# Performance work log

Measured on AMD Instinct MI355X. Metric: run time of the kernel, lower is better.

The kernel has to match this reference:

```python
import jax, jax.numpy as jnp
import numpy as np

H_GRU = 32  # GRU hidden size fixed to 32 in the module


def setup_inputs() -> dict:
    key = jax.random.key(0)
    ks = jax.random.split(key, 12)
    B, C_in, H, W = 64, 64, 48, 160
    C_out = 64
    s_in = 1.0 / np.sqrt(C_in)
    s_h = 1.0 / np.sqrt(H_GRU)
    u = lambda k, shape: jax.random.uniform(k, shape, jnp.float32, -s_h, s_h)
    return {
        "x": jax.random.normal(ks[0], (B, C_in, H, W), jnp.float32),
        "conv_w": jax.random.normal(ks[1], (C_out, C_in), jnp.float32) * s_in,
        "conv_b": jax.random.normal(ks[2], (C_out,), jnp.float32) * s_in,
        "wih_f": u(ks[3], (3 * H_GRU, C_out)),
        "whh_f": u(ks[4], (3 * H_GRU, H_GRU)),
        "bih_f": u(ks[5], (3 * H_GRU,)),
        "bhh_f": u(ks[6], (3 * H_GRU,)),
        "wih_b": u(ks[7], (3 * H_GRU, C_out)),
        "whh_b": u(ks[8], (3 * H_GRU, H_GRU)),
        "bih_b": u(ks[9], (3 * H_GRU,)),
        "bhh_b": u(ks[10], (3 * H_GRU,)),
    }


def _gru_scan(pre, whh, bhh):
    # pre: [N, T, 3H] input-side gate pre-activations (already x@Wih^T + bih)
    N = pre.shape[0]

    def step(h, g):
        gh = h @ whh.T + bhh
        gi_r, gi_z, gi_n = jnp.split(g, 3, axis=-1)
        gh_r, gh_z, gh_n = jnp.split(gh, 3, axis=-1)
        r = jax.nn.sigmoid(gi_r + gh_r)
        z = jax.nn.sigmoid(gi_z + gh_z)
        n = jnp.tanh(gi_n + r * gh_n)
        h_new = (1.0 - z) * n + z * h
        return h_new, h_new

    h0 = jnp.zeros((N, H_GRU), pre.dtype)
    _, ys = jax.lax.scan(step, h0, jnp.swapaxes(pre, 0, 1))  # ys: [T, N, H]
    return jnp.swapaxes(ys, 0, 1)  # [N, T, H]


def reference(x, conv_w, conv_b, wih_f, whh_f, bih_f, bhh_f,
              wih_b, whh_b, bih_b, bhh_b):
    B, C_in, H, W = x.shape
    # 1x1 conv fused with the NCHW->NHWC permute
    y = jnp.einsum('bchw,oc->bhwo', x, conv_w) + conv_b  # [B, H, W, C_out]
    C_out = y.shape[-1]
    seq = y.reshape(B * H, W, C_out)  # GRU batch = B*H, seq_len = W
    # forward direction
    pre_f = jnp.einsum('ntc,gc->ntg', seq, wih_f) + bih_f
    out_f = _gru_scan(pre_f, whh_f, bhh_f)
    # backward direction: scan reversed sequence, then flip output back
    seq_r = seq[:, ::-1, :]
    pre_b = jnp.einsum('ntc,gc->ntg', seq_r, wih_b) + bih_b
    out_b = _gru_scan(pre_b, whh_b, bhh_b)[:, ::-1, :]
    out = jnp.concatenate([out_f, out_b], axis=-1)  # [B*H, W, 2*H_GRU]
    out = out.reshape(B, H, W, 2 * H_GRU)
    return jnp.transpose(out, (0, 3, 1, 2))  # back to NCHW
```

## Files before the change

kernel.cpp:

```cpp
#include <hip/hip_runtime.h>


typedef _Float16 f16x8 __attribute__((ext_vector_type(8)));
typedef _Float16 f16x4 __attribute__((ext_vector_type(4)));
typedef float f32x4 __attribute__((ext_vector_type(4)));

#define HWSTRIDE 7680
#define NCHUNK 10

#define WS_BIAS_OFF 24576

__global__ void fold_weights(const float* __restrict__ conv_w,
                             const float* __restrict__ conv_b,
                             const float* __restrict__ wih_f,
                             const float* __restrict__ bih_f,
                             const float* __restrict__ bhh_f,
                             const float* __restrict__ wih_b,
                             const float* __restrict__ bih_b,
                             const float* __restrict__ bhh_b,
                             void* wsv)
{
    _Float16* W2 = (_Float16*)wsv;
    float* bias = (float*)((char*)wsv + WS_BIAS_OFF);
    const int idx = blockIdx.x * 256 + threadIdx.x;
    if (idx < 12288) {
        const int d = idx / 6144, r = idx % 6144, g = r / 64, c = r % 64;
        const float* wih = d ? wih_b : wih_f;
        float acc = 0.f;
        for (int o = 0; o < 64; ++o) acc += wih[g * 64 + o] * conv_w[o * 64 + c];
        W2[idx] = (_Float16)acc;
    } else if (idx < 12288 + 256) {
        const int e = idx - 12288;
        const int d = e >> 7, rr = e & 127, kind = rr >> 5, j = rr & 31;
        const float* wih = d ? wih_b : wih_f;
        const float* bih = d ? bih_b : bih_f;
        const float* bhh = d ? bhh_b : bhh_f;
        float v;
        if (kind == 0 || kind == 1) {
            const int g = j + kind * 32;
            float b2 = bih[g];
            for (int o = 0; o < 64; ++o) b2 += wih[g * 64 + o] * conv_b[o];
            v = b2 + bhh[g];
        } else if (kind == 2) {
            const int g = j + 64;
            float b2 = bih[g];
            for (int o = 0; o < 64; ++o) b2 += wih[g * 64 + o] * conv_b[o];
            v = b2;
        } else {
            v = bhh[j + 64];
        }
        bias[(d * 4 + kind) * 32 + j] = v;
    }
}

__global__ __launch_bounds__(128, 3)
void gru_fused3(const float* __restrict__ x,
                const float* __restrict__ whh_f,
                const float* __restrict__ whh_b,
                const void* __restrict__ wsv,
                float* __restrict__ out)
{
    __shared__ __align__(16) _Float16 xt[2][2][64][16];
    __shared__ __align__(16) _Float16 s_pre[2][16][2][100];
    __shared__ __align__(16) float s_h[64];

    const int n    = blockIdx.x;
    const int b    = n / 48;
    const int h    = n % 48;
    const int lane = threadIdx.x & 63;
    const int wave = threadIdx.x >> 6;
    const int sw   = blockIdx.x & 1;
    const float* xbase = x + (size_t)b * (64 * HWSTRIDE) + (size_t)h * 160;

    if (wave == sw) {
        const int d0 = lane >> 5, j = lane & 31;
        const float* whh = d0 ? whh_b : whh_f;
        float w[96];
        #pragma unroll
        for (int g3 = 0; g3 < 3; ++g3)
            #pragma unroll
            for (int k4 = 0; k4 < 8; ++k4) {
                const float4 wv = *(const float4*)&whh[(j + 32 * g3) * 32 + k4 * 4];
                w[g3 * 32 + k4 * 4 + 0] = wv.x; w[g3 * 32 + k4 * 4 + 1] = wv.y;
                w[g3 * 32 + k4 * 4 + 2] = wv.z; w[g3 * 32 + k4 * 4 + 3] = wv.w;
            }
        const float* bias = (const float*)((const char*)wsv + WS_BIAS_OFF);
        const float bc_r = bias[(d0 * 4 + 0) * 32 + j];
        const float bc_z = bias[(d0 * 4 + 1) * 32 + j];
        const float b2n  = bias[(d0 * 4 + 2) * 32 + j];
        const float bhn  = bias[(d0 * 4 + 3) * 32 + j];
        float* orow = out + (((size_t)b * 64 + (size_t)(d0 * 32 + j)) * 48 + h) * 160;

        s_h[lane] = 0.f;
        float hcur = 0.f;
        __syncthreads();

        for (int ci = 0; ci < NCHUNK; ++ci) {
            const int buf = ci & 1;
            float hh[16];
            #pragma unroll
            for (int tq = 0; tq < 16; ++tq) {
                const float pr = (float)s_pre[buf][tq][d0][j];
                const float pz = (float)s_pre[buf][tq][d0][j + 32];
                const float pn = (float)s_pre[buf][tq][d0][j + 64];
                float4 hq[8];
                #pragma unroll
                for (int q = 0; q < 8; ++q) hq[q] = ((const float4*)&s_h[d0 * 32])[q];
                const float* hv = (const float*)hq;
                float ar = bc_r, az = bc_z, an = bhn;
                float ar2 = 0.f, az2 = 0.f, an2 = 0.f;
                #pragma unroll
                for (int k = 0; k < 32; k += 2) {
                    const float h0 = hv[k], h1 = hv[k + 1];
                    ar  = fmaf(w[k],      h0, ar );
                    az  = fmaf(w[32 + k], h0, az );
                    an  = fmaf(w[64 + k], h0, an );
                    ar2 = fmaf(w[k + 1],      h1, ar2);
                    az2 = fmaf(w[33 + k],     h1, az2);
                    an2 = fmaf(w[65 + k],     h1, an2);
                }
                const float gr = (ar + ar2) + pr;
                const float gz = (az + az2) + pz;
                const float gn = an + an2;
                const float r = __builtin_amdgcn_rcpf(1.f + __expf(-gr));
                const float z = __builtin_amdgcn_rcpf(1.f + __expf(-gz));
                float ta = (pn + b2n) + r * gn;
                ta = fminf(fmaxf(ta, -15.f), 15.f);
                const float e2 = __expf(2.f * ta);
                const float nn = (e2 - 1.f) * __builtin_amdgcn_rcpf(e2 + 1.f);
                hcur = (1.f - z) * nn + z * hcur;
                s_h[lane] = hcur;
                asm volatile("" ::: "memory");
                hh[tq] = hcur;
            }
            if (d0 == 0) {
                #pragma unroll
                for (int q = 0; q < 4; ++q)
                    *(float4*)&orow[ci * 16 + q * 4] =
                        make_float4(hh[q*4], hh[q*4+1], hh[q*4+2], hh[q*4+3]);
            } else {
                const int base = 144 - ci * 16;
                #pragma unroll
                for (int q = 0; q < 4; ++q)
                    *(float4*)&orow[base + q * 4] =
                        make_float4(hh[15-q*4], hh[14-q*4], hh[13-q*4], hh[12-q*4]);
            }
            __syncthreads();
        }
    } else {
        const _Float16* W2 = (const _Float16*)wsv;
        const int t  = lane & 15;
        const int g8 = (lane >> 4) * 8;
        const int g4 = (lane >> 4) * 4;
        f16x8 A[2][6][2];
        #pragma unroll
        for (int d = 0; d < 2; ++d)
            #pragma unroll
            for (int gt = 0; gt < 6; ++gt)
                #pragma unroll
                for (int kt = 0; kt < 2; ++kt)
                    A[d][gt][kt] = *(const f16x8*)&W2[(d * 96 + gt * 16 + t) * 64 + kt * 32 + g8];

        const int sc = lane >> 2, stq = lane & 3;

        auto stage_dir = [&](int cc, int d, float4* v, bool issue) {
            const int w0 = d ? (144 - cc * 16) : (cc * 16);
            if (issue) {
                #pragma unroll
                for (int k = 0; k < 4; ++k)
                    v[k] = *(const float4*)(xbase + (size_t)(sc + 16 * k) * HWSTRIDE + w0 + stq * 4);
            } else {
                #pragma unroll
                for (int k = 0; k < 4; ++k) {
                    f16x4 p;
                    p[0] = (_Float16)v[k].x; p[1] = (_Float16)v[k].y;
                    p[2] = (_Float16)v[k].z; p[3] = (_Float16)v[k].w;
                    *(f16x4*)&xt[cc & 1][d][sc + 16 * k][stq * 4] = p;
                }
            }
        };
        auto project_dir = [&](int cn, int d) {
            const int buf = cn & 1;
            const _Float16* xr = &xt[buf][d][0][0];
            f16x8 bf0, bf1;
            #pragma unroll
            for (int e = 0; e < 8; ++e) {
                bf0[e] = xr[(g8 + e) * 16 + t];
                bf1[e] = xr[(32 + g8 + e) * 16 + t];
            }
            const int row = d ? (15 - t) : t;
            #pragma unroll
            for (int gt = 0; gt < 6; ++gt) {
                f32x4 acc = {0.f, 0.f, 0.f, 0.f};
                acc = __builtin_amdgcn_mfma_f32_16x16x32_f16(A[d][gt][0], bf0, acc, 0, 0, 0);
                acc = __builtin_amdgcn_mfma_f32_16x16x32_f16(A[d][gt][1], bf1, acc, 0, 0, 0);
                f16x4 o;
                o[0] = (_Float16)acc[0]; o[1] = (_Float16)acc[1];
                o[2] = (_Float16)acc[2]; o[3] = (_Float16)acc[3];
                *(f16x4*)&s_pre[buf][row][d][gt * 16 + g4] = o;
            }
        };

        {
            float4 v[4];
            stage_dir(0, 0, v, true);  stage_dir(0, 0, v, false);
            stage_dir(0, 1, v, true);  stage_dir(0, 1, v, false);
            stage_dir(1, 0, v, true);  stage_dir(1, 0, v, false);
            stage_dir(1, 1, v, true);  stage_dir(1, 1, v, false);
            project_dir(0, 0);
            project_dir(0, 1);
        }
        __syncthreads();

        for (int ci = 0; ci < NCHUNK; ++ci) {
            const int cn = ci + 1, cs = ci + 2;
            float4 va[4], vb[4];
            if (cs < NCHUNK) stage_dir(cs, 0, va, true);
            if (cn < NCHUNK) project_dir(cn, 0);
            if (cs < NCHUNK) { stage_dir(cs, 0, va, false); stage_dir(cs, 1, vb, true); }
            if (cn < NCHUNK) project_dir(cn, 1);
            if (cs < NCHUNK) stage_dir(cs, 1, vb, false);
            __syncthreads();
        }
    }
}

extern "C" void kernel_launch(void* const* d_in, const int* in_sizes, int n_in,
                              void* d_out, int out_size, void* d_ws, size_t ws_size,
                              hipStream_t stream) {
    (void)in_sizes; (void)n_in; (void)ws_size; (void)out_size;
    fold_weights<<<dim3(49), dim3(256), 0, stream>>>(
        (const float*)d_in[1],
        (const float*)d_in[2],
        (const float*)d_in[3],
        (const float*)d_in[5],
        (const float*)d_in[6],
        (const float*)d_in[7],
        (const float*)d_in[9],
        (const float*)d_in[10],
        d_ws);
    gru_fused3<<<dim3(3072), dim3(128), 0, stream>>>(
        (const float*)d_in[0],
        (const float*)d_in[4],
        (const float*)d_in[8],
        d_ws,
        (float*)d_out);
}
```

Measured before the change: 186.9 us.

## Split GRU into single-wave blocks per direction with K-split recurrence

Replaces the two-wave block (one recurrence wave plus one projection/staging wave) with one 64-lane block per sequence and direction, which doubles the grid. Each block stages its own input and runs its own MFMA projection between chunks. The recurrent matvec is split over two half-waves, each summing half of K, and the halves are combined with a cross-lane shuffle. This halves the register weights per lane and removes the block barriers. The cost is that projection now runs serially with the recurrence inside one wave instead of overlapping with it, and f16 conversion now uses packed RTZ.

```diff
diff --git a/kernel.cpp b/kernel.cpp
--- a/kernel.cpp
+++ b/kernel.cpp
@@ -2,12 +2,11 @@
 
 
 typedef _Float16 f16x8 __attribute__((ext_vector_type(8)));
-typedef _Float16 f16x4 __attribute__((ext_vector_type(4)));
+typedef __fp16   pk16  __attribute__((ext_vector_type(2)));
 typedef float f32x4 __attribute__((ext_vector_type(4)));
 
 #define HWSTRIDE 7680
 #define NCHUNK 10
-
 #define WS_BIAS_OFF 24576
 
 __global__ void fold_weights(const float* __restrict__ conv_w,
@@ -53,174 +52,155 @@
     }
 }
 
-__global__ __launch_bounds__(128, 3)
-void gru_fused3(const float* __restrict__ x,
+__global__ __launch_bounds__(64, 3)
+void gru_fused4(const float* __restrict__ x,
                 const float* __restrict__ whh_f,
                 const float* __restrict__ whh_b,
                 const void* __restrict__ wsv,
                 float* __restrict__ out)
 {
-    __shared__ __align__(16) _Float16 xt[2][2][64][16];
-    __shared__ __align__(16) _Float16 s_pre[2][16][2][100];
-    __shared__ __align__(16) float s_h[64];
-
-    const int n    = blockIdx.x;
+    __shared__ __align__(16) _Float16 xt[64][18];
+    __shared__ __align__(16) _Float16 s_pre[16][104];
+    __shared__ __align__(16) float s_h[32];
+
+    const int d    = blockIdx.x & 1;
+    const int n    = blockIdx.x >> 1;
     const int b    = n / 48;
     const int h    = n % 48;
-    const int lane = threadIdx.x & 63;
-    const int wave = threadIdx.x >> 6;
-    const int sw   = blockIdx.x & 1;
+    const int lane = threadIdx.x;
+    const int kh   = lane >> 5;
+    const int j    = lane & 31;
+    const int t16  = lane & 15;
+    const int g8   = (lane >> 4) * 8;
+    const int sc   = lane >> 2;
+    const int stq  = lane & 3;
+
     const float* xbase = x + (size_t)b * (64 * HWSTRIDE) + (size_t)h * 160;
 
-    if (wave == sw) {
-        const int d0 = lane >> 5, j = lane & 31;
-        const float* whh = d0 ? whh_b : whh_f;
-        float w[96];
-        #pragma unroll
-        for (int g3 = 0; g3 < 3; ++g3)
+    const _Float16* W2 = (const _Float16*)wsv + (size_t)d * 96 * 64;
+    f16x8 A[6][2];
+    #pragma unroll
+    for (int gt = 0; gt < 6; ++gt)
+        #pragma unroll
+        for (int kt = 0; kt < 2; ++kt)
+            A[gt][kt] = *(const f16x8*)&W2[(gt * 16 + t16) * 64 + kt * 32 + g8];
+
+    const float* whh = d ? whh_b : whh_f;
+    float w[48];
+    #pragma unroll
+    for (int g = 0; g < 3; ++g)
+        #pragma unroll
+        for (int q = 0; q < 4; ++q) {
+            const float4 wv = *(const float4*)&whh[(j + 32 * g) * 32 + kh * 16 + q * 4];
+            w[g * 16 + q * 4 + 0] = wv.x; w[g * 16 + q * 4 + 1] = wv.y;
+            w[g * 16 + q * 4 + 2] = wv.z; w[g * 16 + q * 4 + 3] = wv.w;
+        }
+    const float* bias = (const float*)((const char*)wsv + WS_BIAS_OFF);
+    const float bc_r = bias[(d * 4 + 0) * 32 + j];
+    const float bc_z = bias[(d * 4 + 1) * 32 + j];
+    const float b2n  = bias[(d * 4 + 2) * 32 + j];
+    const float bhn  = bias[(d * 4 + 3) * 32 + j];
+
+    float* orow = out + (((size_t)b * 64 + (size_t)(d * 32 + j)) * 48 + h) * 160;
+
+    float4 pf[4];
+    auto issue_pf = [&](int cc) {
+        const int w0 = d ? (144 - cc * 16) : (cc * 16);
+        #pragma unroll
+        for (int k = 0; k < 4; ++k)
+            pf[k] = *(const float4*)(xbase + (size_t)(sc + 16 * k) * HWSTRIDE + w0 + stq * 4);
+    };
+    auto write_xt = [&]() {
+        #pragma unroll
+        for (int k = 0; k < 4; ++k) {
+            pk16 lo = __builtin_amdgcn_cvt_pkrtz(pf[k].x, pf[k].y);
+            pk16 hi = __builtin_amdgcn_cvt_pkrtz(pf[k].z, pf[k].w);
+            *(pk16*)&xt[sc + 16 * k][stq * 4]     = lo;
+            *(pk16*)&xt[sc + 16 * k][stq * 4 + 2] = hi;
+        }
+    };
+    auto project = [&]() {
+        f16x8 bf0, bf1;
+        #pragma unroll
+        for (int e = 0; e < 8; ++e) {
+            bf0[e] = xt[g8 + e][t16];
+            bf1[e] = xt[32 + g8 + e][t16];
+        }
+        const int row = d ? (15 - t16) : t16;
+        #pragma unroll
+        for (int gt = 0; gt < 6; ++gt) {
+            f32x4 acc = {0.f, 0.f, 0.f, 0.f};
+            acc = __builtin_amdgcn_mfma_f32_16x16x32_f16(A[gt][0], bf0, acc, 0, 0, 0);
+            acc = __builtin_amdgcn_mfma_f32_16x16x32_f16(A[gt][1], bf1, acc, 0, 0, 0);
+            pk16 o0 = __builtin_amdgcn_cvt_pkrtz(acc[0], acc[1]);
+            pk16 o1 = __builtin_amdgcn_cvt_pkrtz(acc[2], acc[3]);
+            *(pk16*)&s_pre[row][gt * 16 + (lane >> 4) * 4]     = o0;
+            *(pk16*)&s_pre[row][gt * 16 + (lane >> 4) * 4 + 2] = o1;
+        }
+    };
+
+    issue_pf(0);
+    write_xt();
+    issue_pf(1);
+    project();
+    if (kh == 0) s_h[j] = 0.f;
+    float hcur = 0.f;
+
+    for (int ci = 0; ci < NCHUNK; ++ci) {
+        float hh[8];
+        #pragma unroll
+        for (int s = 0; s < 16; ++s) {
+            const float pr = (float)s_pre[s][j];
+            const float pz = (float)s_pre[s][j + 32];
+            const float pn = (float)s_pre[s][j + 64];
+            float4 h4[4];
             #pragma unroll
-            for (int k4 = 0; k4 < 8; ++k4) {
-                const float4 wv = *(const float4*)&whh[(j + 32 * g3) * 32 + k4 * 4];
-                w[g3 * 32 + k4 * 4 + 0] = wv.x; w[g3 * 32 + k4 * 4 + 1] = wv.y;
-                w[g3 * 32 + k4 * 4 + 2] = wv.z; w[g3 * 32 + k4 * 4 + 3] = wv.w;
+            for (int q = 0; q < 4; ++q) h4[q] = ((const float4*)&s_h[16 * kh])[q];
+            const float* hv = (const float*)h4;
+            float ar0 = 0.f, az0 = 0.f, an0 = 0.f;
+            float ar1 = 0.f, az1 = 0.f, an1 = 0.f;
+            #pragma unroll
+            for (int k = 0; k < 16; k += 2) {
+                const float h0 = hv[k], h1 = hv[k + 1];
+                ar0 = fmaf(w[k],          h0, ar0);
+                az0 = fmaf(w[16 + k],     h0, az0);
+                an0 = fmaf(w[32 + k],     h0, an0);
+                ar1 = fmaf(w[k + 1],      h1, ar1);
+                az1 = fmaf(w[17 + k],     h1, az1);
+                an1 = fmaf(w[33 + k],     h1, an1);
             }
-        const float* bias = (const float*)((const char*)wsv + WS_BIAS_OFF);
-        const float bc_r = bias[(d0 * 4 + 0) * 32 + j];
-        const float bc_z = bias[(d0 * 4 + 1) * 32 + j];
-        const float b2n  = bias[(d0 * 4 + 2) * 32 + j];
-        const float bhn  = bias[(d0 * 4 + 3) * 32 + j];
-        float* orow = out + (((size_t)b * 64 + (size_t)(d0 * 32 + j)) * 48 + h) * 160;
-
-        s_h[lane] = 0.f;
-        float hcur = 0.f;
-        __syncthreads();
-
-        for (int ci = 0; ci < NCHUNK; ++ci) {
-            const int buf = ci & 1;
-            float hh[16];
-            #pragma unroll
-            for (int tq = 0; tq < 16; ++tq) {
-                const float pr = (float)s_pre[buf][tq][d0][j];
-                const float pz = (float)s_pre[buf][tq][d0][j + 32];
-                const float pn = (float)s_pre[buf][tq][d0][j + 64];
-                float4 hq[8];
-                #pragma unroll
-                for (int q = 0; q < 8; ++q) hq[q] = ((const float4*)&s_h[d0 * 32])[q];
-                const float* hv = (const float*)hq;
-                float ar = bc_r, az = bc_z, an = bhn;
-                float ar2 = 0.f, az2 = 0.f, an2 = 0.f;
-                #pragma unroll
-                for (int k = 0; k < 32; k += 2) {
-                    const float h0 = hv[k], h1 = hv[k + 1];
-                    ar  = fmaf(w[k],      h0, ar );
-                    az  = fmaf(w[32 + k], h0, az );
-                    an  = fmaf(w[64 + k], h0, an );
-                    ar2 = fmaf(w[k + 1],      h1, ar2);
-                    az2 = fmaf(w[33 + k],     h1, az2);
-                    an2 = fmaf(w[65 + k],     h1, an2);
-                }
-                const float gr = (ar + ar2) + pr;
-                const float gz = (az + az2) + pz;
-                const float gn = an + an2;
-                const float r = __builtin_amdgcn_rcpf(1.f + __expf(-gr));
-                const float z = __builtin_amdgcn_rcpf(1.f + __expf(-gz));
-                float ta = (pn + b2n) + r * gn;
-                ta = fminf(fmaxf(ta, -15.f), 15.f);
-                const float e2 = __expf(2.f * ta);
-                const float nn = (e2 - 1.f) * __builtin_amdgcn_rcpf(e2 + 1.f);
-                hcur = (1.f - z) * nn + z * hcur;
-                s_h[lane] = hcur;
-                asm volatile("" ::: "memory");
-                hh[tq] = hcur;
-            }
-            if (d0 == 0) {
-                #pragma unroll
-                for (int q = 0; q < 4; ++q)
-                    *(float4*)&orow[ci * 16 + q * 4] =
-                        make_float4(hh[q*4], hh[q*4+1], hh[q*4+2], hh[q*4+3]);
-            } else {
-                const int base = 144 - ci * 16;
-                #pragma unroll
-                for (int q = 0; q < 4; ++q)
-                    *(float4*)&orow[base + q * 4] =
-                        make_float4(hh[15-q*4], hh[14-q*4], hh[13-q*4], hh[12-q*4]);
-            }
-            __syncthreads();
-        }
-    } else {
-        const _Float16* W2 = (const _Float16*)wsv;
-        const int t  = lane & 15;
-        const int g8 = (lane >> 4) * 8;
-        const int g4 = (lane >> 4) * 4;
-        f16x8 A[2][6][2];
-        #pragma unroll
-        for (int d = 0; d < 2; ++d)
-            #pragma unroll
-            for (int gt = 0; gt < 6; ++gt)
-                #pragma unroll
-                for (int kt = 0; kt < 2; ++kt)
-                    A[d][gt][kt] = *(const f16x8*)&W2[(d * 96 + gt * 16 + t) * 64 + kt * 32 + g8];
-
-        const int sc = lane >> 2, stq = lane & 3;
-
-        auto stage_dir = [&](int cc, int d, float4* v, bool issue) {
-            const int w0 = d ? (144 - cc * 16) : (cc * 16);
-            if (issue) {
-                #pragma unroll
-                for (int k = 0; k < 4; ++k)
-                    v[k] = *(const float4*)(xbase + (size_t)(sc + 16 * k) * HWSTRIDE + w0 + stq * 4);
-            } else {
-                #pragma unroll
-                for (int k = 0; k < 4; ++k) {
-                    f16x4 p;
-                    p[0] = (_Float16)v[k].x; p[1] = (_Float16)v[k].y;
-                    p[2] = (_Float16)v[k].z; p[3] = (_Float16)v[k].w;
-                    *(f16x4*)&xt[cc & 1][d][sc + 16 * k][stq * 4] = p;
-                }
-            }
-        };
-        auto project_dir = [&](int cn, int d) {
-            const int buf = cn & 1;
-            const _Float16* xr = &xt[buf][d][0][0];
-            f16x8 bf0, bf1;
-            #pragma unroll
-            for (int e = 0; e < 8; ++e) {
-                bf0[e] = xr[(g8 + e) * 16 + t];
-                bf1[e] = xr[(32 + g8 + e) * 16 + t];
-            }
-            const int row = d ? (15 - t) : t;
-            #pragma unroll
-            for (int gt = 0; gt < 6; ++gt) {
-                f32x4 acc = {0.f, 0.f, 0.f, 0.f};
-                acc = __builtin_amdgcn_mfma_f32_16x16x32_f16(A[d][gt][0], bf0, acc, 0, 0, 0);
-                acc = __builtin_amdgcn_mfma_f32_16x16x32_f16(A[d][gt][1], bf1, acc, 0, 0, 0);
-                f16x4 o;
-                o[0] = (_Float16)acc[0]; o[1] = (_Float16)acc[1];
-                o[2] = (_Float16)acc[2]; o[3] = (_Float16)acc[3];
-                *(f16x4*)&s_pre[buf][row][d][gt * 16 + g4] = o;
-            }
-        };
-
-        {
-            float4 v[4];
-            stage_dir(0, 0, v, true);  stage_dir(0, 0, v, false);
-            stage_dir(0, 1, v, true);  stage_dir(0, 1, v, false);
-            stage_dir(1, 0, v, true);  stage_dir(1, 0, v, false);
-            stage_dir(1, 1, v, true);  stage_dir(1, 1, v, false);
-            project_dir(0, 0);
-            project_dir(0, 1);
-        }
-        __syncthreads();
-
-        for (int ci = 0; ci < NCHUNK; ++ci) {
-            const int cn = ci + 1, cs = ci + 2;
-            float4 va[4], vb[4];
-            if (cs < NCHUNK) stage_dir(cs, 0, va, true);
-            if (cn < NCHUNK) project_dir(cn, 0);
-            if (cs < NCHUNK) { stage_dir(cs, 0, va, false); stage_dir(cs, 1, vb, true); }
-            if (cn < NCHUNK) project_dir(cn, 1);
-            if (cs < NCHUNK) stage_dir(cs, 1, vb, false);
-            __syncthreads();
+            float ar = ar0 + ar1, az = az0 + az1, an = an0 + an1;
+            ar += __shfl_xor(ar, 32);
+            az += __shfl_xor(az, 32);
+            an += __shfl_xor(an, 32);
+            const float gr = ar + pr + bc_r;
+            const float gz = az + pz + bc_z;
+            const float r = __builtin_amdgcn_rcpf(1.f + __expf(-gr));
+            const float z = __builtin_amdgcn_rcpf(1.f + __expf(-gz));
+            float ta = (pn + b2n) + r * (an + bhn);
+            ta = fminf(fmaxf(ta, -15.f), 15.f);
+            const float e2 = __expf(2.f * ta);
+            const float nn = (e2 - 1.f) * __builtin_amdgcn_rcpf(e2 + 1.f);
+            hcur = (1.f - z) * nn + z * hcur;
+            if (kh == 0) s_h[j] = hcur;
+            asm volatile("" ::: "memory");
+            if ((s >> 3) == kh) hh[s & 7] = hcur;
+        }
+        if (d == 0) {
+            *(float4*)&orow[ci * 16 + 8 * kh] =
+                make_float4(hh[0], hh[1], hh[2], hh[3]);
+            *(float4*)&orow[ci * 16 + 8 * kh + 4] =
+                make_float4(hh[4], hh[5], hh[6], hh[7]);
+        } else {
+            *(float4*)&orow[156 - ci * 16 - 8 * kh] =
+                make_float4(hh[3], hh[2], hh[1], hh[0]);
+            *(float4*)&orow[152 - ci * 16 - 8 * kh] =
+                make_float4(hh[7], hh[6], hh[5], hh[4]);
+        }
+        if (ci < NCHUNK - 1) {
+            write_xt();
+            if (ci < NCHUNK - 2) issue_pf(ci + 2);
+            project();
         }
     }
 }
@@ -239,7 +219,7 @@
         (const float*)d_in[9],
         (const float*)d_in[10],
         d_ws);
-    gru_fused3<<<dim3(3072), dim3(128), 0, stream>>>(
+    gru_fused4<<<dim3(6144), dim3(64), 0, stream>>>(
         (const float*)d_in[0],
         (const float*)d_in[4],
         (const float*)d_in[8],
```

After: 188.7 us. No clear change (+1.0%).
